# Kernel optimization log

Hardware: AMD Instinct MI355X
Metric: run time of the kernel (lower is better)

The kernel has to match this reference:

```python
import jax, jax.numpy as jnp
import numpy as np

D_MODEL = 1024
HEADS = 16
D_HEAD = D_MODEL // HEADS


def relative_shift(score):
    # score: [b, h, n, 2n-1] -> [b, h, n, n] via the pad/reshape skew trick
    b, h, n, r = score.shape  # r == 2n - 1
    score = jnp.pad(score, ((0, 0), (0, 0), (0, 0), (1, 0)))  # [b,h,n,2n]
    score = score.reshape(b, h, n * 2 * n)[:, :, n:].reshape(b, h, n, 2 * n - 1)
    return score[..., :n]


def setup_inputs() -> dict:
    key = jax.random.key(0)
    ks = jax.random.split(key, 16)
    b, n, d = 4, 1024, D_MODEL
    s = 1.0 / np.sqrt(d)
    inp = {
        "query": jax.random.normal(ks[0], (b, n, d), jnp.float32),
        "key": jax.random.normal(ks[1], (b, n, d), jnp.float32),
        "value": jax.random.normal(ks[2], (b, n, d), jnp.float32),
        "pos_emb": jax.random.normal(ks[3], (b, 2 * n - 1, d), jnp.float32),
        "Wq": jax.random.normal(ks[4], (d, d), jnp.float32) * s,
        "bq": jnp.zeros((d,), jnp.float32),
        "Wk": jax.random.normal(ks[5], (d, d), jnp.float32) * s,
        "bk": jnp.zeros((d,), jnp.float32),
        "Wv": jax.random.normal(ks[6], (d, d), jnp.float32) * s,
        "bv": jnp.zeros((d,), jnp.float32),
        "Wo": jax.random.normal(ks[7], (d, d), jnp.float32) * s,
        "bo": jnp.zeros((d,), jnp.float32),
        "Wp": jax.random.normal(ks[8], (d, d), jnp.float32) * s,  # pos_proj, no bias
        "u_bias": jax.random.normal(ks[9], (HEADS, D_HEAD), jnp.float32) * 0.05,
        "v_bias": jax.random.normal(ks[10], (HEADS, D_HEAD), jnp.float32) * 0.05,
    }
    return inp


def reference(query, key, value, pos_emb, Wq, bq, Wk, bk, Wv, bv, Wo, bo, Wp, u_bias, v_bias):
    b, n, d = query.shape
    h, dh = HEADS, D_HEAD
    q = (query @ Wq + bq).reshape(b, n, h, dh)            # [b,n,h,dh]
    k = (key @ Wk + bk).reshape(b, n, h, dh)              # [b,n,h,dh]
    v = (value @ Wv + bv).reshape(b, n, h, dh)            # [b,n,h,dh]
    p = (pos_emb @ Wp).reshape(b, 2 * n - 1, h, dh)       # [b,2n-1,h,dh]

    content_score = jnp.einsum('bnhd,bmhd->bhnm', q + u_bias, k)   # [b,h,n,n]
    pos_score = jnp.einsum('bnhd,brhd->bhnr', q + v_bias, p)        # [b,h,n,2n-1]
    pos_score = relative_shift(pos_score)                           # [b,h,n,n]

    score = (content_score + pos_score) / jnp.sqrt(jnp.asarray(d, score_dtype := query.dtype))
    attn = jax.nn.softmax(score, axis=-1)                 # dropout p=0.0 -> identity
    out = jnp.einsum('bhnm,bmhd->bnhd', attn, v).reshape(b, n, d)
    out = out @ Wo + bo
    return out, attn, content_score, pos_score
```

## Files before the change

### kernel.cpp

```cpp
#include <hip/hip_runtime.h>
#include <hip/hip_bf16.h>

typedef __bf16 bf16;
typedef __attribute__((ext_vector_type(8))) __bf16 bf16x8;
typedef __attribute__((ext_vector_type(4))) float f32x4;

#define DEV static __device__ __forceinline__

namespace {

constexpr int B = 4, N = 1024, D = 1024, H = 16, DH = 64;
constexpr int R2 = 2 * N - 1;
constexpr int BH = B * H;
constexpr float SCL = 0.03125f;

DEV bf16 f2b(float x) {
  unsigned u = __builtin_bit_cast(unsigned, x);
  unsigned r = u + 0x7FFFu + ((u >> 16) & 1u);
  unsigned short h = (unsigned short)(r >> 16);
  return __builtin_bit_cast(bf16, h);
}

DEV unsigned cvtpk(float lo, float hi) {
  unsigned r;
  asm("v_cvt_pk_bf16_f32 %0, %1, %2" : "=v"(r) : "v"(lo), "v"(hi));
  return r;
}

DEV bf16x8 cvt8pk(float4 a, float4 b) {
  union { unsigned u[4]; bf16x8 v; } r;
  r.u[0] = cvtpk(a.x, a.y); r.u[1] = cvtpk(a.z, a.w);
  r.u[2] = cvtpk(b.x, b.y); r.u[3] = cvtpk(b.z, b.w);
  return r.v;
}

DEV f32x4 mfma16(bf16x8 a, bf16x8 b, f32x4 c) {
  return __builtin_amdgcn_mfma_f32_16x16x32_bf16(a, b, c, 0, 0, 0);
}

DEV void nt_store4(float4 v, float* p) {
  f32x4 x = {v.x, v.y, v.z, v.w};
  __builtin_nontemporal_store(x, reinterpret_cast<f32x4*>(p));
}

DEV void block_sync_lds() {
  __builtin_amdgcn_sched_barrier(0);
  asm volatile("s_waitcnt lgkmcnt(0)" ::: "memory");
  __builtin_amdgcn_s_barrier();
  __builtin_amdgcn_sched_barrier(0);
}

__global__ __launch_bounds__(256) void transpose_cast_w(
    const float* __restrict__ w0, const float* __restrict__ w1,
    const float* __restrict__ w2, const float* __restrict__ w3,
    const float* __restrict__ w4, bf16* __restrict__ t0, bf16* __restrict__ t1,
    bf16* __restrict__ t2, bf16* __restrict__ t3, bf16* __restrict__ t4) {
  const float* src; bf16* dst;
  switch (blockIdx.z) {
    case 0: src = w0; dst = t0; break;
    case 1: src = w1; dst = t1; break;
    case 2: src = w2; dst = t2; break;
    case 3: src = w3; dst = t3; break;
    default: src = w4; dst = t4; break;
  }
  __shared__ float tile[64][65];
  const int k0 = blockIdx.y * 64, n0 = blockIdx.x * 64;
  const int t = threadIdx.x, r = t >> 2, c0 = (t & 3) * 16;
  const float4* sp = reinterpret_cast<const float4*>(src + (size_t)(k0 + r) * D + n0 + c0);
#pragma unroll
  for (int q = 0; q < 4; ++q) {
    float4 v = sp[q];
    tile[r][c0 + q * 4 + 0] = v.x; tile[r][c0 + q * 4 + 1] = v.y;
    tile[r][c0 + q * 4 + 2] = v.z; tile[r][c0 + q * 4 + 3] = v.w;
  }
  __syncthreads();
  union { unsigned u[8]; uint4 q[2]; } pk;
#pragma unroll
  for (int e = 0; e < 8; ++e)
    pk.u[e] = cvtpk(tile[c0 + 2 * e][r], tile[c0 + 2 * e + 1][r]);
  uint4* dp = reinterpret_cast<uint4*>(dst + (size_t)(n0 + r) * D + k0 + c0);
  dp[0] = pk.q[0]; dp[1] = pk.q[1];
}

enum { M_QUV = 0, M_HEAD = 1, M_P = 2, M_OUT = 3 };

template <bool ABF>
DEV void proj_core(char* smem, const void* __restrict__ Av,
                   const bf16* __restrict__ Bt, int M, int mt, int nt, int mode,
                   const float* __restrict__ bias, const float* __restrict__ ubp,
                   const float* __restrict__ vbp, bf16* __restrict__ dst0,
                   bf16* __restrict__ dst1, float* __restrict__ outf) {
  bf16* As = (bf16*)smem;
  bf16* Bs = (bf16*)(smem + 16384);
  float* ep = (float*)smem;
  const int t = threadIdx.x;
  const int m0 = mt * 128, n0 = nt * 128;
  const int lane = t & 63, w = t >> 6;
  const int wi = w >> 1, wj = w & 1;
  const int fr = lane & 15, g = lane >> 4;
  f32x4 acc[4][4] = {};

  int rowc[4], ccc[4], rmc[4];
#pragma unroll
  for (int it = 0; it < 4; ++it) {
    const int chunk = it * 256 + t;
    rowc[it] = chunk >> 3; ccc[it] = chunk & 7;
    int rm = m0 + rowc[it]; rmc[it] = rm < M ? rm : M - 1;
  }
  float4 raf[4][2];
  bf16x8 rab[4];
  bf16x8 rbb[4];
  auto loadstep = [&](int k0) {
#pragma unroll
    for (int it = 0; it < 4; ++it) {
      if (ABF) {
        rab[it] = *reinterpret_cast<const bf16x8*>(
            (const bf16*)Av + (size_t)rmc[it] * D + k0 + ccc[it] * 8);
      } else {
        const float4* ap = reinterpret_cast<const float4*>(
            (const float*)Av + (size_t)rmc[it] * D + k0 + ccc[it] * 8);
        raf[it][0] = ap[0]; raf[it][1] = ap[1];
      }
      rbb[it] = *reinterpret_cast<const bf16x8*>(
          Bt + (size_t)(n0 + rowc[it]) * D + k0 + ccc[it] * 8);
    }
  };

  loadstep(0);
  for (int k0 = 0; k0 < D; k0 += 64) {
#pragma unroll
    for (int it = 0; it < 4; ++it) {
      const int row = rowc[it], cc = ccc[it];
      bf16x8 av;
      if (ABF) av = rab[it]; else av = cvt8pk(raf[it][0], raf[it][1]);
      *reinterpret_cast<bf16x8*>(&As[row * 64 + ((cc ^ (row & 7)) << 3)]) = av;
      *reinterpret_cast<bf16x8*>(&Bs[row * 64 + ((cc ^ (row & 7)) << 3)]) =
          rbb[it];
    }
    block_sync_lds();
    if (k0 + 64 < D) loadstep(k0 + 64);
#pragma unroll
    for (int ks = 0; ks < 2; ++ks) {
      bf16x8 fa[4], fb[4];
#pragma unroll
      for (int i = 0; i < 4; ++i) {
        const int row = wi * 64 + i * 16 + fr;
        fa[i] = *reinterpret_cast<const bf16x8*>(
            &As[row * 64 + (((ks * 4 + g) ^ (row & 7)) << 3)]);
      }
#pragma unroll
      for (int j = 0; j < 4; ++j) {
        const int row = wj * 64 + j * 16 + fr;
        fb[j] = *reinterpret_cast<const bf16x8*>(
            &Bs[row * 64 + (((ks * 4 + g) ^ (row & 7)) << 3)]);
      }
#pragma unroll
      for (int i = 0; i < 4; ++i)
#pragma unroll
        for (int j = 0; j < 4; ++j) acc[i][j] = mfma16(fa[i], fb[j], acc[i][j]);
    }
    block_sync_lds();
  }
#pragma unroll
  for (int p = 0; p < 2; ++p) {
    block_sync_lds();
    if (wi == p) {
#pragma unroll
      for (int i = 0; i < 4; ++i)
#pragma unroll
        for (int j = 0; j < 4; ++j)
#pragma unroll
          for (int q = 0; q < 4; ++q)
            ep[(i * 16 + g * 4 + q) * 132 + wj * 64 + j * 16 + fr] =
                acc[i][j][q];
    }
    block_sync_lds();
    const int lr = t >> 2, cl = (t & 3) * 32;
    const int m = m0 + p * 64 + lr;
    if (m < M) {
      float v[32];
#pragma unroll
      for (int kk = 0; kk < 8; ++kk) {
        const float4 f =
            *reinterpret_cast<const float4*>(&ep[lr * 132 + cl + kk * 4]);
        v[kk * 4 + 0] = f.x; v[kk * 4 + 1] = f.y;
        v[kk * 4 + 2] = f.z; v[kk * 4 + 3] = f.w;
      }
      const int cg0 = n0 + cl;
      if (mode == M_OUT) {
        float* op = outf + (size_t)m * D + cg0;
#pragma unroll
        for (int kk = 0; kk < 8; ++kk) {
          float4 f = {v[kk * 4] + bias[cg0 + kk * 4],
                      v[kk * 4 + 1] + bias[cg0 + kk * 4 + 1],
                      v[kk * 4 + 2] + bias[cg0 + kk * 4 + 2],
                      v[kk * 4 + 3] + bias[cg0 + kk * 4 + 3]};
          nt_store4(f, op + kk * 4);
        }
      } else if (mode == M_P) {
        const int b_ = m / R2, r_ = m - b_ * R2;
        const int h_ = cg0 >> 6, dh0 = cg0 & 63;
        bf16* dp = dst0 + (((size_t)(b_ * H + h_)) * R2 + r_) * DH + dh0;
        unsigned pk[16];
#pragma unroll
        for (int e = 0; e < 16; ++e) pk[e] = cvtpk(v[2 * e], v[2 * e + 1]);
#pragma unroll
        for (int kk = 0; kk < 4; ++kk)
          reinterpret_cast<uint4*>(dp)[kk] =
              *reinterpret_cast<const uint4*>(&pk[kk * 4]);
      } else {
        const int b_ = m >> 10, ii = m & (N - 1);
        const int h_ = cg0 >> 6, dh0 = cg0 & 63;
        const size_t o = (((size_t)(b_ * H + h_)) * N + ii) * DH + dh0;
        if (mode == M_QUV) {
          unsigned pku[16], pkv[16];
#pragma unroll
          for (int e = 0; e < 16; ++e) {
            const float b0 = bias[cg0 + 2 * e], b1 = bias[cg0 + 2 * e + 1];
            pku[e] = cvtpk(v[2 * e] + b0 + ubp[cg0 + 2 * e],
                           v[2 * e + 1] + b1 + ubp[cg0 + 2 * e + 1]);
            pkv[e] = cvtpk(v[2 * e] + b0 + vbp[cg0 + 2 * e],
                           v[2 * e + 1] + b1 + vbp[cg0 + 2 * e + 1]);
          }
#pragma unroll
          for (int kk = 0; kk < 4; ++kk) {
            reinterpret_cast<uint4*>(dst0 + o)[kk] =
                *reinterpret_cast<const uint4*>(&pku[kk * 4]);
            reinterpret_cast<uint4*>(dst1 + o)[kk] =
                *reinterpret_cast<const uint4*>(&pkv[kk * 4]);
          }
        } else {
          unsigned pk[16];
#pragma unroll
          for (int e = 0; e < 16; ++e)
            pk[e] = cvtpk(v[2 * e] + bias[cg0 + 2 * e],
                          v[2 * e + 1] + bias[cg0 + 2 * e + 1]);
#pragma unroll
          for (int kk = 0; kk < 4; ++kk)
            reinterpret_cast<uint4*>(dst0 + o)[kk] =
                *reinterpret_cast<const uint4*>(&pk[kk * 4]);
        }
      }
    }
  }
}

__global__ __launch_bounds__(256, 2) void proj_qkvp(
    const float* __restrict__ query, const float* __restrict__ key,
    const float* __restrict__ value, const float* __restrict__ pos_emb,
    const bf16* __restrict__ Wqt, const bf16* __restrict__ Wkt,
    const bf16* __restrict__ Wvt, const bf16* __restrict__ Wpt,
    const float* __restrict__ bq, const float* __restrict__ bk,
    const float* __restrict__ bv, const float* __restrict__ ub,
    const float* __restrict__ vbp, bf16* __restrict__ Qu,
    bf16* __restrict__ Qv, bf16* __restrict__ Kb, bf16* __restrict__ Vb,
    bf16* __restrict__ Pb) {
  __shared__ __align__(16) char smem[34048];
  const int z = blockIdx.z, x = blockIdx.x, y = blockIdx.y;
  const int nt = y & 7;
  const int mt = x * 4 + (y >> 3);
  switch (z) {
    case 0:
      proj_core<false>(smem, query, Wqt, B * N, mt, nt, M_QUV, bq, ub, vbp, Qu,
                       Qv, nullptr);
      break;
    case 1:
      proj_core<false>(smem, key, Wkt, B * N, mt, nt, M_HEAD, bk, nullptr,
                       nullptr, Kb, nullptr, nullptr);
      break;
    case 2:
      proj_core<false>(smem, value, Wvt, B * N, mt, nt, M_HEAD, bv, nullptr,
                       nullptr, Vb, nullptr, nullptr);
      break;
    case 3:
      proj_core<false>(smem, pos_emb, Wpt, B * R2, mt, nt, M_P, nullptr,
                       nullptr, nullptr, Pb, nullptr, nullptr);
      break;
    default:
      proj_core<false>(smem, pos_emb, Wpt, B * R2, 32 + mt, nt, M_P, nullptr,
                       nullptr, nullptr, Pb, nullptr, nullptr);
      break;
  }
}

__global__ __launch_bounds__(256, 2) void proj_out(const bf16* __restrict__ OA,
                                                   const bf16* __restrict__ Wot,
                                                   const float* __restrict__ bo,
                                                   float* __restrict__ outF) {
  __shared__ __align__(16) char smem[34048];
  const int nt = blockIdx.y & 7;
  const int mt = blockIdx.x * 4 + (blockIdx.y >> 3);
  proj_core<true>(smem, OA, Wot, B * N, mt, nt, M_OUT, bo, nullptr, nullptr,
                  nullptr, nullptr, outF);
}

__global__ __launch_bounds__(256) void transpose_v(const bf16* __restrict__ V,
                                                   bf16* __restrict__ Vt) {
  __shared__ bf16 tile[64][72];
  const int bh = blockIdx.y, k0 = blockIdx.x * 64;
  const int t = threadIdx.x, r = t >> 2, c0 = (t & 3) * 16;
  const bf16x8* sp =
      reinterpret_cast<const bf16x8*>(V + ((size_t)bh * N + k0 + r) * DH + c0);
  *reinterpret_cast<bf16x8*>(&tile[r][c0]) = sp[0];
  *reinterpret_cast<bf16x8*>(&tile[r][c0 + 8]) = sp[1];
  __syncthreads();
  union { bf16 h[16]; uint4 u[2]; } pk;
#pragma unroll
  for (int e = 0; e < 16; ++e) pk.h[e] = tile[c0 + e][r];
  uint4* dp = reinterpret_cast<uint4*>(Vt + ((size_t)bh * DH + r) * N + k0 + c0);
  dp[0] = pk.u[0]; dp[1] = pk.u[1];
}

constexpr int RB = 16;

DEV int SIDX(int r, int c) {
  return r * 1024 + (((c >> 2) ^ (r & 7)) << 2) + (c & 3);
}

__global__ __launch_bounds__(512, 4) void fused_attn(
    const bf16* __restrict__ Qu, const bf16* __restrict__ Qv,
    const bf16* __restrict__ Kb, const bf16* __restrict__ Pb,
    const bf16* __restrict__ Vt, float* __restrict__ cont,
    float* __restrict__ posS, float* __restrict__ attn,
    bf16* __restrict__ OA) {
  __shared__ float sc[RB * 1024];
  __shared__ float red[1024];
  const int bid0 = blockIdx.y * 64 + blockIdx.x;
  const int bid = (bid0 & 7) * 512 + (bid0 >> 3);
  const int bh = bid >> 6, i0 = (bid & 63) * RB;
  const int t = threadIdx.x, lane = t & 63, w = t >> 6;
  const int fr = lane & 15, g = lane >> 4, kg = g * 8;

  {
    const bf16* Qub = Qu + ((size_t)bh * N + i0) * DH;
    const bf16* Kbh = Kb + (size_t)bh * N * DH;
    const bf16x8 fa0 = *reinterpret_cast<const bf16x8*>(Qub + (size_t)fr * DH + kg);
    const bf16x8 fa1 = *reinterpret_cast<const bf16x8*>(Qub + (size_t)fr * DH + 32 + kg);
#pragma unroll
    for (int tt = 0; tt < 8; ++tt) {
      const int ct = (w * 8 + tt) * 16;
      const bf16x8 fb0 =
          *reinterpret_cast<const bf16x8*>(Kbh + (size_t)(ct + fr) * DH + kg);
      const bf16x8 fb1 =
          *reinterpret_cast<const bf16x8*>(Kbh + (size_t)(ct + fr) * DH + 32 + kg);
      f32x4 acc = {};
      acc = mfma16(fa0, fb0, acc);
      acc = mfma16(fa1, fb1, acc);
      const int c = ct + fr;
#pragma unroll
      for (int q = 0; q < 4; ++q) sc[SIDX(g * 4 + q, c)] = acc[q];
    }
  }
  block_sync_lds();

  float4 xc[2][4];
#pragma unroll
  for (int rr2 = 0; rr2 < 2; ++rr2) {
    const int r = w * 2 + rr2;
#pragma unroll
    for (int k = 0; k < 4; ++k) {
      const int ch = (k * 64 + lane) ^ (r & 7);
      xc[rr2][k] = *reinterpret_cast<const float4*>(&sc[r * 1024 + ch * 4]);
    }
  }
  block_sync_lds();

  {
    float* contb = cont + ((size_t)bh * N + i0) * N;
#pragma unroll
    for (int rr2 = 0; rr2 < 2; ++rr2) {
      const int r = w * 2 + rr2;
#pragma unroll
      for (int k = 0; k < 4; ++k)
        nt_store4(xc[rr2][k], contb + (size_t)r * N + (k * 64 + lane) * 4);
    }
    const bf16* Qvb = Qv + ((size_t)bh * N + i0) * DH;
    const bf16* Pbh = Pb + (size_t)bh * R2 * DH;
    const bf16x8 fa0 = *reinterpret_cast<const bf16x8*>(Qvb + (size_t)fr * DH + kg);
    const bf16x8 fa1 = *reinterpret_cast<const bf16x8*>(Qvb + (size_t)fr * DH + 32 + kg);
    const int Rlo = (N - RB) - i0;
    for (int tt = w; tt < 65; tt += 8) {
      const int rr = Rlo + tt * 16 + fr;
      const int rc = rr < R2 ? rr : R2 - 1;
      const bf16x8 fb0 =
          *reinterpret_cast<const bf16x8*>(Pbh + (size_t)rc * DH + kg);
      const bf16x8 fb1 =
          *reinterpret_cast<const bf16x8*>(Pbh + (size_t)rc * DH + 32 + kg);
      f32x4 acc = {};
      acc = mfma16(fa0, fb0, acc);
      acc = mfma16(fa1, fb1, acc);
#pragma unroll
      for (int q = 0; q < 4; ++q) {
        const int r = g * 4 + q;
        const int jj = rr - (N - 1) + i0 + r;
        if (rr < R2 && jj >= 0 && jj < N) sc[SIDX(r, jj)] = acc[q];
      }
    }
  }
  block_sync_lds();

  {
    float* posb = posS + ((size_t)bh * N + i0) * N;
    float* attnb = attn + ((size_t)bh * N + i0) * N;
#pragma unroll
    for (int rr2 = 0; rr2 < 2; ++rr2) {
      const int r = w * 2 + rr2;
      float4 xp[4], x[4];
      int ch[4];
#pragma unroll
      for (int k = 0; k < 4; ++k) {
        ch[k] = (k * 64 + lane) ^ (r & 7);
        xp[k] = *reinterpret_cast<const float4*>(&sc[r * 1024 + ch[k] * 4]);
      }
      float mx = -1e30f;
#pragma unroll
      for (int k = 0; k < 4; ++k) {
        nt_store4(xp[k], posb + (size_t)r * N + (k * 64 + lane) * 4);
        x[k].x = xc[rr2][k].x + xp[k].x; x[k].y = xc[rr2][k].y + xp[k].y;
        x[k].z = xc[rr2][k].z + xp[k].z; x[k].w = xc[rr2][k].w + xp[k].w;
        mx = fmaxf(mx, fmaxf(fmaxf(x[k].x, x[k].y), fmaxf(x[k].z, x[k].w)));
      }
#pragma unroll
      for (int o = 32; o; o >>= 1) mx = fmaxf(mx, __shfl_xor(mx, o));
      float sum = 0.f;
#pragma unroll
      for (int k = 0; k < 4; ++k) {
        x[k].x = __expf((x[k].x - mx) * SCL);
        x[k].y = __expf((x[k].y - mx) * SCL);
        x[k].z = __expf((x[k].z - mx) * SCL);
        x[k].w = __expf((x[k].w - mx) * SCL);
        sum += x[k].x + x[k].y + x[k].z + x[k].w;
      }
#pragma unroll
      for (int o = 32; o; o >>= 1) sum += __shfl_xor(sum, o);
      const float inv = 1.0f / sum;
#pragma unroll
      for (int k = 0; k < 4; ++k) {
        float4 y = {x[k].x * inv, x[k].y * inv, x[k].z * inv, x[k].w * inv};
        nt_store4(y, attnb + (size_t)r * N + (k * 64 + lane) * 4);
        *reinterpret_cast<float4*>(&sc[r * 1024 + ch[k] * 4]) = y;
      }
    }
  }
  block_sync_lds();

  {
    const bf16* Vbh = Vt + (size_t)bh * DH * N;
    const int wi = w >> 2, wj = w & 3;
    f32x4 acc = {};
    for (int kt = wi * 16; kt < wi * 16 + 16; ++kt) {
      const int p0 = (kt * 8 + g * 2) ^ (fr & 7);
      const float4 a0 = *reinterpret_cast<const float4*>(&sc[fr * 1024 + p0 * 4]);
      const float4 a1 =
          *reinterpret_cast<const float4*>(&sc[fr * 1024 + (p0 ^ 1) * 4]);
      const bf16x8 fb = *reinterpret_cast<const bf16x8*>(
          Vbh + (size_t)(wj * 16 + fr) * N + kt * 32 + kg);
      acc = mfma16(cvt8pk(a0, a1), fb, acc);
    }
    if (wi == 1) *reinterpret_cast<f32x4*>(&red[(wj * 64 + lane) * 4]) = acc;
    block_sync_lds();
    if (wi == 0) {
      const f32x4 o = *reinterpret_cast<const f32x4*>(&red[(wj * 64 + lane) * 4]);
      const int b_ = bh >> 4, h_ = bh & 15;
#pragma unroll
      for (int q = 0; q < 4; ++q) {
        const int row = i0 + g * 4 + q;
        const int dh = wj * 16 + fr;
        OA[((size_t)b_ * N + row) * D + h_ * DH + dh] = f2b(acc[q] + o[q]);
      }
    }
  }
}

}

extern "C" void kernel_launch(void* const* d_in, const int* in_sizes, int n_in,
                              void* d_out, int out_size, void* d_ws,
                              size_t ws_size, hipStream_t stream) {
  (void)in_sizes; (void)n_in; (void)out_size; (void)ws_size;
  const float* query = (const float*)d_in[0];
  const float* key = (const float*)d_in[1];
  const float* value = (const float*)d_in[2];
  const float* pos_emb = (const float*)d_in[3];
  const float* Wq = (const float*)d_in[4];
  const float* bq = (const float*)d_in[5];
  const float* Wk = (const float*)d_in[6];
  const float* bk = (const float*)d_in[7];
  const float* Wv = (const float*)d_in[8];
  const float* bv = (const float*)d_in[9];
  const float* Wo = (const float*)d_in[10];
  const float* bo = (const float*)d_in[11];
  const float* Wp = (const float*)d_in[12];
  const float* ub = (const float*)d_in[13];
  const float* vb = (const float*)d_in[14];

  float* outF = (float*)d_out;
  float* attn = outF + (size_t)B * N * D;
  float* cont = attn + (size_t)BH * N * N;
  float* posS = cont + (size_t)BH * N * N;

  char* wsp = (char*)d_ws;
  auto alloc = [&](size_t elems) {
    bf16* p = (bf16*)wsp;
    wsp += elems * sizeof(bf16);
    return p;
  };
  bf16* Qu = alloc((size_t)BH * N * DH);
  bf16* Qv = alloc((size_t)BH * N * DH);
  bf16* Kb = alloc((size_t)BH * N * DH);
  bf16* Vb = alloc((size_t)BH * N * DH);
  bf16* Vt = alloc((size_t)BH * DH * N);
  bf16* Pb = alloc((size_t)BH * R2 * DH);
  bf16* OA = alloc((size_t)B * N * D);
  bf16* Wqt = alloc((size_t)D * D);
  bf16* Wkt = alloc((size_t)D * D);
  bf16* Wvt = alloc((size_t)D * D);
  bf16* Wpt = alloc((size_t)D * D);
  bf16* Wot = alloc((size_t)D * D);

  dim3 blk(256);
  transpose_cast_w<<<dim3(16, 16, 5), blk, 0, stream>>>(Wq, Wk, Wv, Wp, Wo, Wqt,
                                                        Wkt, Wvt, Wpt, Wot);
  proj_qkvp<<<dim3(8, 32, 5), blk, 0, stream>>>(query, key, value, pos_emb,
                                                Wqt, Wkt, Wvt, Wpt, bq, bk, bv,
                                                ub, vb, Qu, Qv, Kb, Vb, Pb);
  transpose_v<<<dim3(16, 64), blk, 0, stream>>>(Vb, Vt);
  fused_attn<<<dim3(64, 64), dim3(512), 0, stream>>>(Qu, Qv, Kb, Pb, Vt, cont,
                                                     posS, attn, OA);
  proj_out<<<dim3(8, 32), blk, 0, stream>>>(OA, Wot, bo, outF);
}
```

Baseline: 350.0 us.

## Pre-cast activations to bf16, double-buffer GEMM via direct global-to-LDS loads, fuse V transpose

```diff
diff --git a/kernel.cpp b/kernel.cpp
--- a/kernel.cpp
+++ b/kernel.cpp
@@ -13,6 +13,7 @@
 constexpr int R2 = 2 * N - 1;
 constexpr int BH = B * H;
 constexpr float SCL = 0.03125f;
+constexpr int MP = B * R2;
 
 DEV bf16 f2b(float x) {
   unsigned u = __builtin_bit_cast(unsigned, x);
@@ -50,95 +51,114 @@
   __builtin_amdgcn_sched_barrier(0);
 }
 
-__global__ __launch_bounds__(256) void transpose_cast_w(
+DEV void sync_stage() {
+  __builtin_amdgcn_sched_barrier(0);
+  asm volatile("s_waitcnt vmcnt(0) lgkmcnt(0)" ::: "memory");
+  __builtin_amdgcn_s_barrier();
+  __builtin_amdgcn_sched_barrier(0);
+}
+
+typedef const unsigned int __attribute__((address_space(1)))* gas_t;
+typedef unsigned int __attribute__((address_space(3)))* las_t;
+DEV void gload16(const bf16* g, bf16* l) {
+  __builtin_amdgcn_global_load_lds((gas_t)g, (las_t)l, 16, 0, 0);
+}
+
+__global__ __launch_bounds__(256) void prep(
     const float* __restrict__ w0, const float* __restrict__ w1,
     const float* __restrict__ w2, const float* __restrict__ w3,
     const float* __restrict__ w4, bf16* __restrict__ t0, bf16* __restrict__ t1,
-    bf16* __restrict__ t2, bf16* __restrict__ t3, bf16* __restrict__ t4) {
-  const float* src; bf16* dst;
-  switch (blockIdx.z) {
-    case 0: src = w0; dst = t0; break;
-    case 1: src = w1; dst = t1; break;
-    case 2: src = w2; dst = t2; break;
-    case 3: src = w3; dst = t3; break;
-    default: src = w4; dst = t4; break;
-  }
-  __shared__ float tile[64][65];
-  const int k0 = blockIdx.y * 64, n0 = blockIdx.x * 64;
-  const int t = threadIdx.x, r = t >> 2, c0 = (t & 3) * 16;
-  const float4* sp = reinterpret_cast<const float4*>(src + (size_t)(k0 + r) * D + n0 + c0);
-#pragma unroll
-  for (int q = 0; q < 4; ++q) {
-    float4 v = sp[q];
-    tile[r][c0 + q * 4 + 0] = v.x; tile[r][c0 + q * 4 + 1] = v.y;
-    tile[r][c0 + q * 4 + 2] = v.z; tile[r][c0 + q * 4 + 3] = v.w;
-  }
-  __syncthreads();
-  union { unsigned u[8]; uint4 q[2]; } pk;
-#pragma unroll
-  for (int e = 0; e < 8; ++e)
-    pk.u[e] = cvtpk(tile[c0 + 2 * e][r], tile[c0 + 2 * e + 1][r]);
-  uint4* dp = reinterpret_cast<uint4*>(dst + (size_t)(n0 + r) * D + k0 + c0);
-  dp[0] = pk.q[0]; dp[1] = pk.q[1];
-}
-
-enum { M_QUV = 0, M_HEAD = 1, M_P = 2, M_OUT = 3 };
-
-template <bool ABF>
-DEV void proj_core(char* smem, const void* __restrict__ Av,
+    bf16* __restrict__ t2, bf16* __restrict__ t3, bf16* __restrict__ t4,
+    const float* __restrict__ query, const float* __restrict__ key,
+    const float* __restrict__ value, const float* __restrict__ pos_emb,
+    bf16* __restrict__ qb, bf16* __restrict__ kb, bf16* __restrict__ vb,
+    bf16* __restrict__ pb) {
+  const int z = blockIdx.z;
+  if (z < 5) {
+    const float* src; bf16* dst;
+    switch (z) {
+      case 0: src = w0; dst = t0; break;
+      case 1: src = w1; dst = t1; break;
+      case 2: src = w2; dst = t2; break;
+      case 3: src = w3; dst = t3; break;
+      default: src = w4; dst = t4; break;
+    }
+    __shared__ float tile[64][65];
+    const int k0 = blockIdx.y * 64, n0 = blockIdx.x * 64;
+    const int t = threadIdx.x, r = t >> 2, c0 = (t & 3) * 16;
+    const float4* sp =
+        reinterpret_cast<const float4*>(src + (size_t)(k0 + r) * D + n0 + c0);
+#pragma unroll
+    for (int q = 0; q < 4; ++q) {
+      float4 v = sp[q];
+      tile[r][c0 + q * 4 + 0] = v.x; tile[r][c0 + q * 4 + 1] = v.y;
+      tile[r][c0 + q * 4 + 2] = v.z; tile[r][c0 + q * 4 + 3] = v.w;
+    }
+    __syncthreads();
+    union { unsigned u[8]; uint4 q[2]; } pk;
+#pragma unroll
+    for (int e = 0; e < 8; ++e)
+      pk.u[e] = cvtpk(tile[c0 + 2 * e][r], tile[c0 + 2 * e + 1][r]);
+    uint4* dp = reinterpret_cast<uint4*>(dst + (size_t)(n0 + r) * D + k0 + c0);
+    dp[0] = pk.q[0]; dp[1] = pk.q[1];
+    return;
+  }
+  const float* src; bf16* dst; int nch, real;
+  switch (z) {
+    case 5: src = query;   dst = qb; nch = 524288;  real = 524288;  break;
+    case 6: src = key;     dst = kb; nch = 524288;  real = 524288;  break;
+    case 7: src = value;   dst = vb; nch = 524288;  real = 524288;  break;
+    default: src = pos_emb; dst = pb; nch = 1048576; real = 1048064; break;
+  }
+  const int tid = (blockIdx.y * 16 + blockIdx.x) * 256 + threadIdx.x;
+  for (int c = tid; c < nch; c += 65536) {
+    if (c >= real) {
+      uint4 zz = {0, 0, 0, 0};
+      *reinterpret_cast<uint4*>(dst + (size_t)c * 8) = zz;
+    } else {
+      const float4* ap = reinterpret_cast<const float4*>(src + (size_t)c * 8);
+      *reinterpret_cast<bf16x8*>(dst + (size_t)c * 8) = cvt8pk(ap[0], ap[1]);
+    }
+  }
+}
+
+enum { M_QUV = 0, M_HEAD = 1, M_P = 2, M_OUT = 3, M_V = 4 };
+
+DEV void proj_core(char* smem, const bf16* __restrict__ A,
                    const bf16* __restrict__ Bt, int M, int mt, int nt, int mode,
                    const float* __restrict__ bias, const float* __restrict__ ubp,
                    const float* __restrict__ vbp, bf16* __restrict__ dst0,
                    bf16* __restrict__ dst1, float* __restrict__ outf) {
-  bf16* As = (bf16*)smem;
-  bf16* Bs = (bf16*)(smem + 16384);
+  bf16* Asb[2] = {(bf16*)smem, (bf16*)(smem + 32768)};
+  bf16* Bsb[2] = {(bf16*)(smem + 16384), (bf16*)(smem + 49152)};
   float* ep = (float*)smem;
   const int t = threadIdx.x;
   const int m0 = mt * 128, n0 = nt * 128;
   const int lane = t & 63, w = t >> 6;
   const int wi = w >> 1, wj = w & 1;
   const int fr = lane & 15, g = lane >> 4;
+  const int lr8 = lane >> 3, lc = lane & 7;
+
+  auto stage = [&](int buf, int kt) {
+    const int k0 = kt * 64;
+#pragma unroll
+    for (int i = 0; i < 4; ++i) {
+      const int row = (w * 4 + i) * 8 + lr8;
+      gload16(A + (size_t)(m0 + row) * D + k0 + ((lc ^ (row & 7)) << 3),
+              Asb[buf] + (w * 4 + i) * 512);
+      gload16(Bt + (size_t)(n0 + row) * D + k0 + ((lc ^ (row & 7)) << 3),
+              Bsb[buf] + (w * 4 + i) * 512);
+    }
+  };
+
   f32x4 acc[4][4] = {};
-
-  int rowc[4], ccc[4], rmc[4];
-#pragma unroll
-  for (int it = 0; it < 4; ++it) {
-    const int chunk = it * 256 + t;
-    rowc[it] = chunk >> 3; ccc[it] = chunk & 7;
-    int rm = m0 + rowc[it]; rmc[it] = rm < M ? rm : M - 1;
-  }
-  float4 raf[4][2];
-  bf16x8 rab[4];
-  bf16x8 rbb[4];
-  auto loadstep = [&](int k0) {
-#pragma unroll
-    for (int it = 0; it < 4; ++it) {
-      if (ABF) {
-        rab[it] = *reinterpret_cast<const bf16x8*>(
-            (const bf16*)Av + (size_t)rmc[it] * D + k0 + ccc[it] * 8);
-      } else {
-        const float4* ap = reinterpret_cast<const float4*>(
-            (const float*)Av + (size_t)rmc[it] * D + k0 + ccc[it] * 8);
-        raf[it][0] = ap[0]; raf[it][1] = ap[1];
-      }
-      rbb[it] = *reinterpret_cast<const bf16x8*>(
-          Bt + (size_t)(n0 + rowc[it]) * D + k0 + ccc[it] * 8);
-    }
-  };
-
-  loadstep(0);
-  for (int k0 = 0; k0 < D; k0 += 64) {
-#pragma unroll
-    for (int it = 0; it < 4; ++it) {
-      const int row = rowc[it], cc = ccc[it];
-      bf16x8 av;
-      if (ABF) av = rab[it]; else av = cvt8pk(raf[it][0], raf[it][1]);
-      *reinterpret_cast<bf16x8*>(&As[row * 64 + ((cc ^ (row & 7)) << 3)]) = av;
-      *reinterpret_cast<bf16x8*>(&Bs[row * 64 + ((cc ^ (row & 7)) << 3)]) =
-          rbb[it];
-    }
-    block_sync_lds();
-    if (k0 + 64 < D) loadstep(k0 + 64);
+  stage(0, 0);
+  sync_stage();
+  int cur = 0;
+  for (int kt = 0; kt < 16; ++kt) {
+    if (kt < 15) stage(cur ^ 1, kt + 1);
+    const bf16* As = Asb[cur];
+    const bf16* Bs = Bsb[cur];
 #pragma unroll
     for (int ks = 0; ks < 2; ++ks) {
       bf16x8 fa[4], fb[4];
@@ -159,8 +179,10 @@
 #pragma unroll
         for (int j = 0; j < 4; ++j) acc[i][j] = mfma16(fa[i], fb[j], acc[i][j]);
     }
-    block_sync_lds();
-  }
+    sync_stage();
+    cur ^= 1;
+  }
+
 #pragma unroll
   for (int p = 0; p < 2; ++p) {
     block_sync_lds();
@@ -175,6 +197,27 @@
                 acc[i][j][q];
     }
     block_sync_lds();
+    if (mode == M_V) {
+      const int col = t >> 1, seg = t & 1;
+      const int cg = n0 + col;
+      const int h_ = cg >> 6, dh = cg & 63;
+      const int b_ = m0 >> 10;
+      const int tok0 = (m0 & 1023) + p * 64 + seg * 32;
+      const float bvv = bias[cg];
+      unsigned pk[16];
+#pragma unroll
+      for (int e = 0; e < 16; ++e) {
+        const float v0 = ep[(seg * 32 + 2 * e + 0) * 132 + col] + bvv;
+        const float v1 = ep[(seg * 32 + 2 * e + 1) * 132 + col] + bvv;
+        pk[e] = cvtpk(v0, v1);
+      }
+      bf16* dp = dst0 + ((size_t)(b_ * H + h_) * DH + dh) * N + tok0;
+#pragma unroll
+      for (int kk = 0; kk < 4; ++kk)
+        reinterpret_cast<uint4*>(dp)[kk] =
+            *reinterpret_cast<const uint4*>(&pk[kk * 4]);
+      continue;
+    }
     const int lr = t >> 2, cl = (t & 3) * 32;
     const int m = m0 + p * 64 + lr;
     if (m < M) {
@@ -246,39 +289,39 @@
 }
 
 __global__ __launch_bounds__(256, 2) void proj_qkvp(
-    const float* __restrict__ query, const float* __restrict__ key,
-    const float* __restrict__ value, const float* __restrict__ pos_emb,
+    const bf16* __restrict__ qb, const bf16* __restrict__ kb,
+    const bf16* __restrict__ vbin, const bf16* __restrict__ pbin,
     const bf16* __restrict__ Wqt, const bf16* __restrict__ Wkt,
     const bf16* __restrict__ Wvt, const bf16* __restrict__ Wpt,
     const float* __restrict__ bq, const float* __restrict__ bk,
     const float* __restrict__ bv, const float* __restrict__ ub,
     const float* __restrict__ vbp, bf16* __restrict__ Qu,
-    bf16* __restrict__ Qv, bf16* __restrict__ Kb, bf16* __restrict__ Vb,
+    bf16* __restrict__ Qv, bf16* __restrict__ Kb, bf16* __restrict__ Vt,
     bf16* __restrict__ Pb) {
-  __shared__ __align__(16) char smem[34048];
+  __shared__ __align__(16) char smem[65536];
   const int z = blockIdx.z, x = blockIdx.x, y = blockIdx.y;
   const int nt = y & 7;
   const int mt = x * 4 + (y >> 3);
   switch (z) {
     case 0:
-      proj_core<false>(smem, query, Wqt, B * N, mt, nt, M_QUV, bq, ub, vbp, Qu,
-                       Qv, nullptr);
+      proj_core(smem, qb, Wqt, B * N, mt, nt, M_QUV, bq, ub, vbp, Qu, Qv,
+                nullptr);
       break;
     case 1:
-      proj_core<false>(smem, key, Wkt, B * N, mt, nt, M_HEAD, bk, nullptr,
-                       nullptr, Kb, nullptr, nullptr);
+      proj_core(smem, kb, Wkt, B * N, mt, nt, M_HEAD, bk, nullptr, nullptr, Kb,
+                nullptr, nullptr);
       break;
     case 2:
-      proj_core<false>(smem, value, Wvt, B * N, mt, nt, M_HEAD, bv, nullptr,
-                       nullptr, Vb, nullptr, nullptr);
+      proj_core(smem, vbin, Wvt, B * N, mt, nt, M_V, bv, nullptr, nullptr, Vt,
+                nullptr, nullptr);
       break;
     case 3:
-      proj_core<false>(smem, pos_emb, Wpt, B * R2, mt, nt, M_P, nullptr,
-                       nullptr, nullptr, Pb, nullptr, nullptr);
+      proj_core(smem, pbin, Wpt, MP, mt, nt, M_P, nullptr, nullptr, nullptr,
+                Pb, nullptr, nullptr);
       break;
     default:
-      proj_core<false>(smem, pos_emb, Wpt, B * R2, 32 + mt, nt, M_P, nullptr,
-                       nullptr, nullptr, Pb, nullptr, nullptr);
+      proj_core(smem, pbin, Wpt, MP, 32 + mt, nt, M_P, nullptr, nullptr,
+                nullptr, Pb, nullptr, nullptr);
       break;
   }
 }
@@ -287,28 +330,11 @@
                                                    const bf16* __restrict__ Wot,
                                                    const float* __restrict__ bo,
                                                    float* __restrict__ outF) {
-  __shared__ __align__(16) char smem[34048];
+  __shared__ __align__(16) char smem[65536];
   const int nt = blockIdx.y & 7;
   const int mt = blockIdx.x * 4 + (blockIdx.y >> 3);
-  proj_core<true>(smem, OA, Wot, B * N, mt, nt, M_OUT, bo, nullptr, nullptr,
-                  nullptr, nullptr, outF);
-}
-
-__global__ __launch_bounds__(256) void transpose_v(const bf16* __restrict__ V,
-                                                   bf16* __restrict__ Vt) {
-  __shared__ bf16 tile[64][72];
-  const int bh = blockIdx.y, k0 = blockIdx.x * 64;
-  const int t = threadIdx.x, r = t >> 2, c0 = (t & 3) * 16;
-  const bf16x8* sp =
-      reinterpret_cast<const bf16x8*>(V + ((size_t)bh * N + k0 + r) * DH + c0);
-  *reinterpret_cast<bf16x8*>(&tile[r][c0]) = sp[0];
-  *reinterpret_cast<bf16x8*>(&tile[r][c0 + 8]) = sp[1];
-  __syncthreads();
-  union { bf16 h[16]; uint4 u[2]; } pk;
-#pragma unroll
-  for (int e = 0; e < 16; ++e) pk.h[e] = tile[c0 + e][r];
-  uint4* dp = reinterpret_cast<uint4*>(Vt + ((size_t)bh * DH + r) * N + k0 + c0);
-  dp[0] = pk.u[0]; dp[1] = pk.u[1];
+  proj_core(smem, OA, Wot, B * N, mt, nt, M_OUT, bo, nullptr, nullptr, nullptr,
+            nullptr, outF);
 }
 
 constexpr int RB = 16;
@@ -508,10 +534,13 @@
   bf16* Qu = alloc((size_t)BH * N * DH);
   bf16* Qv = alloc((size_t)BH * N * DH);
   bf16* Kb = alloc((size_t)BH * N * DH);
-  bf16* Vb = alloc((size_t)BH * N * DH);
   bf16* Vt = alloc((size_t)BH * DH * N);
   bf16* Pb = alloc((size_t)BH * R2 * DH);
   bf16* OA = alloc((size_t)B * N * D);
+  bf16* qb = alloc((size_t)B * N * D);
+  bf16* kb = alloc((size_t)B * N * D);
+  bf16* vbB = alloc((size_t)B * N * D);
+  bf16* pb = alloc((size_t)8192 * D);
   bf16* Wqt = alloc((size_t)D * D);
   bf16* Wkt = alloc((size_t)D * D);
   bf16* Wvt = alloc((size_t)D * D);
@@ -519,12 +548,12 @@
   bf16* Wot = alloc((size_t)D * D);
 
   dim3 blk(256);
-  transpose_cast_w<<<dim3(16, 16, 5), blk, 0, stream>>>(Wq, Wk, Wv, Wp, Wo, Wqt,
-                                                        Wkt, Wvt, Wpt, Wot);
-  proj_qkvp<<<dim3(8, 32, 5), blk, 0, stream>>>(query, key, value, pos_emb,
-                                                Wqt, Wkt, Wvt, Wpt, bq, bk, bv,
-                                                ub, vb, Qu, Qv, Kb, Vb, Pb);
-  transpose_v<<<dim3(16, 64), blk, 0, stream>>>(Vb, Vt);
+  prep<<<dim3(16, 16, 9), blk, 0, stream>>>(Wq, Wk, Wv, Wp, Wo, Wqt, Wkt, Wvt,
+                                            Wpt, Wot, query, key, value,
+                                            pos_emb, qb, kb, vbB, pb);
+  proj_qkvp<<<dim3(8, 32, 5), blk, 0, stream>>>(qb, kb, vbB, pb, Wqt, Wkt, Wvt,
+                                                Wpt, bq, bk, bv, ub, vb, Qu,
+                                                Qv, Kb, Vt, Pb);
   fused_attn<<<dim3(64, 64), dim3(512), 0, stream>>>(Qu, Qv, Kb, Pb, Vt, cont,
                                                      posS, attn, OA);
   proj_out<<<dim3(8, 32), blk, 0, stream>>>(OA, Wot, bo, outF);
```

New measurement: 376.7 us. 7.6% more time.
